# Performance work log

Measured on AMD Instinct MI355X. Metric: run time of the kernel, lower is better.

Reference implementation:

```python
import jax, jax.numpy as jnp
import numpy as np

N_NODES = 50000
N_EDGES = 800000
IN_FEATS = 256
HIDDEN = 128
OUT_FEATS = 64


def setup_inputs() -> dict:
    key = jax.random.key(0)
    k1, k2, k3, k4, k5 = jax.random.split(key, 5)
    x = jax.random.normal(k1, (N_NODES, IN_FEATS), dtype=jnp.float32)
    src = jax.random.randint(k2, (N_EDGES,), 0, N_NODES, dtype=jnp.int64)
    dst = jax.random.randint(k3, (N_EDGES,), 0, N_NODES, dtype=jnp.int64)
    # Glorot-ish init for linear weights (DGL GraphConv uses xavier_uniform)
    W1 = jax.random.normal(k4, (IN_FEATS, HIDDEN), dtype=jnp.float32) / np.sqrt(IN_FEATS)
    W2 = jax.random.normal(k5, (HIDDEN, OUT_FEATS), dtype=jnp.float32) / np.sqrt(HIDDEN)
    b1 = jnp.zeros((HIDDEN,), dtype=jnp.float32)
    b2 = jnp.zeros((OUT_FEATS,), dtype=jnp.float32)
    return {"x": x, "src": src, "dst": dst, "W1": W1, "b1": b1, "W2": W2, "b2": b2}


def _norms(src, dst, n_nodes):
    ones = jnp.ones(src.shape[0], dtype=jnp.float32)
    deg_out = jax.ops.segment_sum(ones, src, num_segments=n_nodes)
    deg_in = jax.ops.segment_sum(ones, dst, num_segments=n_nodes)
    # DGL clamps zero degrees to 1 to avoid inf
    norm_src = jnp.power(jnp.clip(deg_out, 1.0, None), -0.5)  # [N]
    norm_dst = jnp.power(jnp.clip(deg_in, 1.0, None), -0.5)   # [N]
    return norm_src, norm_dst


def _gcn_layer(h, W, b, src, dst, norm_src, norm_dst, n_nodes):
    # norm='both': D_dst^{-1/2} A D_src^{-1/2} (h W) + b
    # multiply by W first (in_feats >= out_feats -> cheaper aggregation)
    m = (h * norm_src[:, None]) @ W            # [N, out]
    agg = jax.ops.segment_sum(m[src], dst, num_segments=n_nodes)  # [N, out]
    return agg * norm_dst[:, None] + b


def reference(x, src, dst, W1, b1, W2, b2):
    n = x.shape[0]
    norm_src, norm_dst = _norms(src, dst, n)
    h = _gcn_layer(x, W1, b1, src, dst, norm_src, norm_dst, n)
    h = jax.nn.relu(h)
    h = _gcn_layer(h, W2, b2, src, dst, norm_src, norm_dst, n)
    return h
```

## Files before the change

kernel.cpp:

```cpp
#include <hip/hip_runtime.h>

#define N_NODES 50000
#define N_EDGES 800000
#define IN_FEATS 256
#define HIDDEN 128
#define OUT_FEATS 64

#define NB 8192
#define NRANGE 7
#define NBT (NRANGE * NB)
#define NCHUNK 64
#define EPC 12500
#define HBLK (NRANGE * NCHUNK)
#define ROWBLK ((N_NODES + 63) / 64)
#define G1BLK (ROWBLK * 2)

typedef _Float16 f16;
typedef _Float16 f16x2 __attribute__((ext_vector_type(2)));
typedef _Float16 f16x8 __attribute__((ext_vector_type(8)));
typedef float f32x4 __attribute__((ext_vector_type(4)));

__global__ __launch_bounds__(256) void hist_gemm_kernel(
    const int* __restrict__ src, const int* __restrict__ dst,
    unsigned* __restrict__ hist_src, unsigned* __restrict__ hist_dst,
    const float* __restrict__ W1, const float* __restrict__ W2,
    f16* __restrict__ W2T, const float* __restrict__ x,
    f16* __restrict__ m1) {
  __shared__ __align__(16) unsigned smem[8448];
  if (blockIdx.x < HBLK) {
    unsigned* ls = smem;
    unsigned* ld2 = smem + NB / 2;
    const int r = blockIdx.x % NRANGE;
    const int c = blockIdx.x / NRANGE;
    const int lo = r * NB;
    for (int i = threadIdx.x; i < NB / 2; i += 256) {
      ls[i] = 0;
      ld2[i] = 0;
    }
    __syncthreads();
    const int4* s4 = (const int4*)(src + c * EPC);
    const int4* d4 = (const int4*)(dst + c * EPC);
    for (int i = threadIdx.x; i < EPC / 4; i += 256) {
      int4 s = s4[i];
      int4 d = d4[i];
      unsigned b;
      b = (unsigned)(s.x - lo); if (b < NB) atomicAdd(&ls[b >> 1], 1u << ((b & 1) << 4));
      b = (unsigned)(s.y - lo); if (b < NB) atomicAdd(&ls[b >> 1], 1u << ((b & 1) << 4));
      b = (unsigned)(s.z - lo); if (b < NB) atomicAdd(&ls[b >> 1], 1u << ((b & 1) << 4));
      b = (unsigned)(s.w - lo); if (b < NB) atomicAdd(&ls[b >> 1], 1u << ((b & 1) << 4));
      b = (unsigned)(d.x - lo); if (b < NB) atomicAdd(&ld2[b >> 1], 1u << ((b & 1) << 4));
      b = (unsigned)(d.y - lo); if (b < NB) atomicAdd(&ld2[b >> 1], 1u << ((b & 1) << 4));
      b = (unsigned)(d.z - lo); if (b < NB) atomicAdd(&ld2[b >> 1], 1u << ((b & 1) << 4));
      b = (unsigned)(d.w - lo); if (b < NB) atomicAdd(&ld2[b >> 1], 1u << ((b & 1) << 4));
    }
    __syncthreads();
    unsigned* hs = hist_src + ((long)c * NBT + lo) / 2;
    unsigned* hd = hist_dst + ((long)c * NBT + lo) / 2;
    for (int i = threadIdx.x; i < NB / 2; i += 256) {
      hs[i] = ls[i];
      hd[i] = ld2[i];
    }
    if (blockIdx.x < 32) {
      int j = blockIdx.x * 256 + threadIdx.x;
      int n = j >> 7, k = j & 127;
      W2T[j] = (f16)W2[k * 64 + n];
    }
  } else {
    f16* Bs = (f16*)smem;
    constexpr int KP = IN_FEATS + 8;
    const int bid = blockIdx.x - HBLK;
    const int cb = bid & 1;
    const int rb = bid >> 1;
    const int col0 = cb * 64;
    const int wave = threadIdx.x >> 6;
    const int lane = threadIdx.x & 63;
    const int m = lane & 15;
    const int q = lane >> 4;
    const int row0 = rb * 64 + wave * 16;

    for (int idx = threadIdx.x; idx < 64 * (IN_FEATS / 2); idx += 256) {
      int k2 = idx >> 6;
      int n = idx & 63;
      float a0 = W1[(2 * k2) * HIDDEN + col0 + n];
      float a1 = W1[(2 * k2 + 1) * HIDDEN + col0 + n];
      f16x2 pk;
      pk[0] = (f16)a0;
      pk[1] = (f16)a1;
      *(f16x2*)(Bs + n * KP + 2 * k2) = pk;
    }
    __syncthreads();

    const int ra = min(row0 + m, N_NODES - 1);
    f32x4 acc[4];
#pragma unroll
    for (int t = 0; t < 4; ++t) acc[t] = (f32x4){0.f, 0.f, 0.f, 0.f};

#pragma unroll
    for (int ki = 0; ki < IN_FEATS / 32; ++ki) {
      const int kb = ki * 32 + q * 8;
      const float* p = x + (long)ra * IN_FEATS + kb;
      float4 u0 = *(const float4*)p;
      float4 u1 = *(const float4*)(p + 4);
      f16x8 a;
      a[0] = (f16)u0.x; a[1] = (f16)u0.y;
      a[2] = (f16)u0.z; a[3] = (f16)u0.w;
      a[4] = (f16)u1.x; a[5] = (f16)u1.y;
      a[6] = (f16)u1.z; a[7] = (f16)u1.w;
#pragma unroll
      for (int t = 0; t < 4; ++t) {
        f16x8 bfr = *(const f16x8*)(Bs + (t * 16 + m) * KP + kb);
        acc[t] = __builtin_amdgcn_mfma_f32_16x16x32_f16(a, bfr, acc[t], 0, 0, 0);
      }
    }

#pragma unroll
    for (int rr = 0; rr < 4; ++rr) {
      int row = row0 + q * 4 + rr;
      if (row < N_NODES) {
#pragma unroll
        for (int t = 0; t < 4; ++t)
          m1[(long)row * HIDDEN + col0 + t * 16 + m] = (f16)acc[t][rr];
      }
    }
  }
}

__global__ __launch_bounds__(256) void reduce_kernel(
    const unsigned* __restrict__ hist_src, unsigned* __restrict__ hist_dst,
    int* __restrict__ deg_in, float* __restrict__ norm_src,
    float* __restrict__ norm_dst, int* __restrict__ partial) {
  const unsigned short* hs = (const unsigned short*)hist_src;
  unsigned short* hd = (unsigned short*)hist_dst;
  int n = blockIdx.x * 256 + threadIdx.x;
  int run = 0;
  if (n < N_NODES) {
    int so = 0;
#pragma unroll 8
    for (int c = 0; c < NCHUNK; ++c) so += hs[(long)c * NBT + n];
    norm_src[n] = rsqrtf((float)max(so, 1));
#pragma unroll 8
    for (int c = 0; c < NCHUNK; ++c) {
      int t = hd[(long)c * NBT + n];
      hd[(long)c * NBT + n] = (unsigned short)run;
      run += t;
    }
    deg_in[n] = run;
    norm_dst[n] = rsqrtf((float)max(run, 1));
  }
  __shared__ int sd[256];
  sd[threadIdx.x] = run;
  __syncthreads();
  for (int s = 128; s > 0; s >>= 1) {
    if (threadIdx.x < s) sd[threadIdx.x] += sd[threadIdx.x + s];
    __syncthreads();
  }
  if (threadIdx.x == 0) partial[blockIdx.x] = sd[0];
}

__global__ __launch_bounds__(256) void scan3(const int* __restrict__ deg,
                                             const int* __restrict__ partial,
                                             int* __restrict__ rowptr) {
  __shared__ int sd[256];
  __shared__ int sp[256];
  const int w = blockIdx.x;
  int pv = (threadIdx.x < 196) ? partial[threadIdx.x] : 0;
  sp[threadIdx.x] = pv;
  __syncthreads();
  for (int off = 1; off < 256; off <<= 1) {
    int t = sp[threadIdx.x] +
            ((threadIdx.x >= off) ? sp[threadIdx.x - off] : 0);
    __syncthreads();
    sp[threadIdx.x] = t;
    __syncthreads();
  }
  const int base = (w == 0) ? 0 : sp[w - 1];
  int i = w * 256 + threadIdx.x;
  int v = (i < N_NODES) ? deg[i] : 0;
  sd[threadIdx.x] = v;
  __syncthreads();
  for (int off = 1; off < 256; off <<= 1) {
    int t = sd[threadIdx.x] +
            ((threadIdx.x >= off) ? sd[threadIdx.x - off] : 0);
    __syncthreads();
    sd[threadIdx.x] = t;
    __syncthreads();
  }
  if (i < N_NODES) rowptr[i] = base + sd[threadIdx.x] - v;
  if (w == 0 && threadIdx.x == 0) rowptr[N_NODES] = N_EDGES;
}

__global__ __launch_bounds__(256) void fill_csr(
    const int* __restrict__ src, const int* __restrict__ dst,
    const int* __restrict__ rowptr, const unsigned* __restrict__ pref32,
    int* __restrict__ col) {
  __shared__ int cur[NB];
  const unsigned short* pref = (const unsigned short*)pref32;
  const int r = blockIdx.x % NRANGE;
  const int c = blockIdx.x / NRANGE;
  const int lo = r * NB;
  for (int i = threadIdx.x; i < NB; i += 256) {
    int n = lo + i;
    cur[i] = (n < N_NODES) ? rowptr[n] + pref[(long)c * NBT + n] : 0;
  }
  __syncthreads();
  const int4* s4 = (const int4*)(src + c * EPC);
  const int4* d4 = (const int4*)(dst + c * EPC);
  for (int i = threadIdx.x; i < EPC / 4; i += 256) {
    int4 s = s4[i];
    int4 d = d4[i];
    unsigned b;
    b = (unsigned)(d.x - lo);
    if (b < NB) col[atomicAdd(&cur[b], 1)] = s.x;
    b = (unsigned)(d.y - lo);
    if (b < NB) col[atomicAdd(&cur[b], 1)] = s.y;
    b = (unsigned)(d.z - lo);
    if (b < NB) col[atomicAdd(&cur[b], 1)] = s.z;
    b = (unsigned)(d.w - lo);
    if (b < NB) col[atomicAdd(&cur[b], 1)] = s.w;
  }
}

template <int K, int NC, int TN, bool FP32IN>
__global__ __launch_bounds__(256) void gemm_mfma(
    const void* __restrict__ Xv, const f16* __restrict__ WT,
    const float* __restrict__ ns, f16* __restrict__ Mout) {
  constexpr int KI = K / 32;
  constexpr int COLBLK = NC / (TN * 16);
  constexpr int KP = K + 8;
  __shared__ f16 Bs[TN * 16 * KP];

  const int cb = blockIdx.x % COLBLK;
  const int rb = blockIdx.x / COLBLK;
  const int col0 = cb * TN * 16;
  const int wave = threadIdx.x >> 6;
  const int lane = threadIdx.x & 63;
  const int m = lane & 15;
  const int q = lane >> 4;
  const int row0 = rb * 64 + wave * 16;

  for (int idx = threadIdx.x; idx < TN * 16 * (K / 8); idx += 256) {
    int n = idx / (K / 8);
    int kk = idx % (K / 8);
    *(f16x8*)(Bs + n * KP + kk * 8) =
        *(const f16x8*)(WT + (long)(col0 + n) * K + kk * 8);
  }
  __syncthreads();

  const int ra = min(row0 + m, N_NODES - 1);
  const float s = FP32IN ? ns[ra] : 0.f;

  f32x4 acc[TN];
#pragma unroll
  for (int t = 0; t < TN; ++t) acc[t] = (f32x4){0.f, 0.f, 0.f, 0.f};

#pragma unroll
  for (int ki = 0; ki < KI; ++ki) {
    const int kb = ki * 32 + q * 8;
    f16x8 a;
    if (FP32IN) {
      const float* X = (const float*)Xv;
      const float* p = X + (long)ra * K + kb;
      float4 u0 = *(const float4*)p;
      float4 u1 = *(const float4*)(p + 4);
      a[0] = (f16)(u0.x * s); a[1] = (f16)(u0.y * s);
      a[2] = (f16)(u0.z * s); a[3] = (f16)(u0.w * s);
      a[4] = (f16)(u1.x * s); a[5] = (f16)(u1.y * s);
      a[6] = (f16)(u1.z * s); a[7] = (f16)(u1.w * s);
    } else {
      const f16* X = (const f16*)Xv;
      a = *(const f16x8*)(X + (long)ra * K + kb);
    }
#pragma unroll
    for (int t = 0; t < TN; ++t) {
      f16x8 b = *(const f16x8*)(Bs + (t * 16 + m) * KP + kb);
      acc[t] = __builtin_amdgcn_mfma_f32_16x16x32_f16(a, b, acc[t], 0, 0, 0);
    }
  }

#pragma unroll
  for (int r = 0; r < 4; ++r) {
    int row = row0 + q * 4 + r;
    if (row < N_NODES) {
#pragma unroll
      for (int t = 0; t < TN; ++t)
        Mout[(long)row * NC + col0 + t * 16 + m] = (f16)acc[t][r];
    }
  }
}

__global__ __launch_bounds__(256) void gather1_kernel(
    const f16* __restrict__ M, const int* __restrict__ rowptr,
    const int* __restrict__ col, const float* __restrict__ nd,
    const float* __restrict__ ns, const float* __restrict__ b,
    f16* __restrict__ out) {
  constexpr int LPR = 16;
  constexpr int EPW = 64 / LPR;
  const int wave = threadIdx.x >> 6;
  const int lane = threadIdx.x & 63;
  const int eg = lane / LPR;
  const int t = lane % LPR;
  const int n = blockIdx.x * 4 + wave;
  if (n >= N_NODES) return;
  const int beg = rowptr[n];
  const int end = rowptr[n + 1];

  float acc[8];
#pragma unroll
  for (int j = 0; j < 8; ++j) acc[j] = 0.f;

  int i = beg + eg;
  for (; i + EPW < end; i += 2 * EPW) {
    int s0 = col[i];
    int s1 = col[i + EPW];
    float n0 = ns[s0];
    float n1 = ns[s1];
    f16x8 v0 = *(const f16x8*)(M + (long)s0 * HIDDEN + t * 8);
    f16x8 v1 = *(const f16x8*)(M + (long)s1 * HIDDEN + t * 8);
#pragma unroll
    for (int j = 0; j < 8; ++j)
      acc[j] += n0 * (float)v0[j] + n1 * (float)v1[j];
  }
  if (i < end) {
    int s0 = col[i];
    float n0 = ns[s0];
    f16x8 v0 = *(const f16x8*)(M + (long)s0 * HIDDEN + t * 8);
#pragma unroll
    for (int j = 0; j < 8; ++j) acc[j] += n0 * (float)v0[j];
  }

#pragma unroll
  for (int m2 = LPR; m2 < 64; m2 <<= 1)
#pragma unroll
    for (int j = 0; j < 8; ++j) acc[j] += __shfl_xor(acc[j], m2, 64);

  if (eg == 0) {
    float s = nd[n];
    float sn = ns[n];
    float4 bb0 = *(const float4*)(b + t * 8);
    float4 bb1 = *(const float4*)(b + t * 8 + 4);
    f16x8 o;
    o[0] = (f16)(fmaxf(acc[0] * s + bb0.x, 0.f) * sn);
    o[1] = (f16)(fmaxf(acc[1] * s + bb0.y, 0.f) * sn);
    o[2] = (f16)(fmaxf(acc[2] * s + bb0.z, 0.f) * sn);
    o[3] = (f16)(fmaxf(acc[3] * s + bb0.w, 0.f) * sn);
    o[4] = (f16)(fmaxf(acc[4] * s + bb1.x, 0.f) * sn);
    o[5] = (f16)(fmaxf(acc[5] * s + bb1.y, 0.f) * sn);
    o[6] = (f16)(fmaxf(acc[6] * s + bb1.z, 0.f) * sn);
    o[7] = (f16)(fmaxf(acc[7] * s + bb1.w, 0.f) * sn);
    *(f16x8*)(out + (long)n * HIDDEN + t * 8) = o;
  }
}

__global__ __launch_bounds__(256) void gather2_kernel(
    const f16* __restrict__ M, const int* __restrict__ rowptr,
    const int* __restrict__ col, const float* __restrict__ nd,
    const float* __restrict__ b, float* __restrict__ out) {
  constexpr int LPR = 8;
  constexpr int EPW = 64 / LPR;
  const int wave = threadIdx.x >> 6;
  const int lane = threadIdx.x & 63;
  const int eg = lane / LPR;
  const int t = lane % LPR;
  const int n = blockIdx.x * 4 + wave;
  if (n >= N_NODES) return;
  const int beg = rowptr[n];
  const int end = rowptr[n + 1];

  float acc[8];
#pragma unroll
  for (int j = 0; j < 8; ++j) acc[j] = 0.f;

  int i = beg + eg;
  for (; i + EPW < end; i += 2 * EPW) {
    int s0 = col[i];
    int s1 = col[i + EPW];
    f16x8 v0 = *(const f16x8*)(M + (long)s0 * OUT_FEATS + t * 8);
    f16x8 v1 = *(const f16x8*)(M + (long)s1 * OUT_FEATS + t * 8);
#pragma unroll
    for (int j = 0; j < 8; ++j) acc[j] += (float)v0[j] + (float)v1[j];
  }
  if (i < end) {
    int s0 = col[i];
    f16x8 v0 = *(const f16x8*)(M + (long)s0 * OUT_FEATS + t * 8);
#pragma unroll
    for (int j = 0; j < 8; ++j) acc[j] += (float)v0[j];
  }

#pragma unroll
  for (int m2 = LPR; m2 < 64; m2 <<= 1)
#pragma unroll
    for (int j = 0; j < 8; ++j) acc[j] += __shfl_xor(acc[j], m2, 64);

  if (eg == 0) {
    float s = nd[n];
    float4 bb0 = *(const float4*)(b + t * 8);
    float4 bb1 = *(const float4*)(b + t * 8 + 4);
    float4 o0, o1;
    o0.x = acc[0] * s + bb0.x;
    o0.y = acc[1] * s + bb0.y;
    o0.z = acc[2] * s + bb0.z;
    o0.w = acc[3] * s + bb0.w;
    o1.x = acc[4] * s + bb1.x;
    o1.y = acc[5] * s + bb1.y;
    o1.z = acc[6] * s + bb1.z;
    o1.w = acc[7] * s + bb1.w;
    *(float4*)(out + (long)n * OUT_FEATS + t * 8) = o0;
    *(float4*)(out + (long)n * OUT_FEATS + t * 8 + 4) = o1;
  }
}

extern "C" void kernel_launch(void* const* d_in, const int* in_sizes, int n_in,
                              void* d_out, int out_size, void* d_ws,
                              size_t ws_size, hipStream_t stream) {
  const float* x = (const float*)d_in[0];
  const int* src = (const int*)d_in[1];
  const int* dst = (const int*)d_in[2];
  const float* W1 = (const float*)d_in[3];
  const float* b1 = (const float*)d_in[4];
  const float* W2 = (const float*)d_in[5];
  const float* b2 = (const float*)d_in[6];
  float* out = (float*)d_out;

  int* wi = (int*)d_ws;
  int* partial = wi;
  int* rowptr = wi + 256;
  int* deg_in = wi + 50260;
  int* col = wi + 100260;
  float* wf = (float*)d_ws + 900260;
  float* norm_src = wf;
  float* norm_dst = wf + 50000;
  f16* fh = (f16*)(wf + 100000);
  f16* W2T = fh;
  f16* m1 = fh + 64 * 128;
  f16* h1p = m1 + (long)50048 * 128;
  f16* m2 = h1p + (long)50048 * 128;

  unsigned* hist_src = (unsigned*)h1p;
  unsigned* hist_dst = hist_src + (long)NCHUNK * NBT / 2;

  const int nb_nodes = (N_NODES + 255) / 256;

  hist_gemm_kernel<<<HBLK + G1BLK, 256, 0, stream>>>(
      src, dst, hist_src, hist_dst, W1, W2, W2T, x, m1);
  reduce_kernel<<<nb_nodes, 256, 0, stream>>>(hist_src, hist_dst, deg_in,
                                              norm_src, norm_dst, partial);
  scan3<<<nb_nodes, 256, 0, stream>>>(deg_in, partial, rowptr);
  fill_csr<<<HBLK, 256, 0, stream>>>(src, dst, rowptr, hist_dst, col);

  gather1_kernel<<<(N_NODES + 3) / 4, 256, 0, stream>>>(m1, rowptr, col,
                                                        norm_dst, norm_src, b1,
                                                        h1p);

  gemm_mfma<HIDDEN, OUT_FEATS, 4, false>
      <<<ROWBLK, 256, 0, stream>>>(h1p, W2T, norm_src, m2);
  gather2_kernel<<<(N_NODES + 3) / 4, 256, 0, stream>>>(m2, rowptr, col,
                                                        norm_dst, b2, out);
}
```

Before: 235.3 us.

## Reuse x row tile across both W1 column halves in fused hist-GEMM kernel

Each GEMM block now handles all 128 output columns for its 64 rows. The x row is loaded and converted to fp16 once into registers, and the block loops over the two 64-column halves of W1, restaging each half into shared memory. This halves the x reads and the block count for the first GEMM. The shared-memory layout drops its padding in favour of an XOR swizzle to avoid bank conflicts. In exchange, each block serializes two W1 staging passes with extra barriers, and more registers are held for the A fragments.

Result: faster. 226.8 us (-3.6%).

```diff
diff --git a/kernel.cpp b/kernel.cpp
--- a/kernel.cpp
+++ b/kernel.cpp
@@ -13,7 +13,6 @@
 #define EPC 12500
 #define HBLK (NRANGE * NCHUNK)
 #define ROWBLK ((N_NODES + 63) / 64)
-#define G1BLK (ROWBLK * 2)
 
 typedef _Float16 f16;
 typedef _Float16 f16x2 __attribute__((ext_vector_type(2)));
@@ -26,7 +25,7 @@
     const float* __restrict__ W1, const float* __restrict__ W2,
     f16* __restrict__ W2T, const float* __restrict__ x,
     f16* __restrict__ m1) {
-  __shared__ __align__(16) unsigned smem[8448];
+  __shared__ __align__(16) unsigned smem[8192];
   if (blockIdx.x < HBLK) {
     unsigned* ls = smem;
     unsigned* ld2 = smem + NB / 2;
@@ -66,60 +65,69 @@
       W2T[j] = (f16)W2[k * 64 + n];
     }
   } else {
-    f16* Bs = (f16*)smem;
-    constexpr int KP = IN_FEATS + 8;
-    const int bid = blockIdx.x - HBLK;
-    const int cb = bid & 1;
-    const int rb = bid >> 1;
-    const int col0 = cb * 64;
+    char* BsBytes = (char*)smem;
+    const int rb = blockIdx.x - HBLK;
     const int wave = threadIdx.x >> 6;
     const int lane = threadIdx.x & 63;
     const int m = lane & 15;
     const int q = lane >> 4;
     const int row0 = rb * 64 + wave * 16;
-
-    for (int idx = threadIdx.x; idx < 64 * (IN_FEATS / 2); idx += 256) {
-      int k2 = idx >> 6;
-      int n = idx & 63;
-      float a0 = W1[(2 * k2) * HIDDEN + col0 + n];
-      float a1 = W1[(2 * k2 + 1) * HIDDEN + col0 + n];
-      f16x2 pk;
-      pk[0] = (f16)a0;
-      pk[1] = (f16)a1;
-      *(f16x2*)(Bs + n * KP + 2 * k2) = pk;
-    }
-    __syncthreads();
-
     const int ra = min(row0 + m, N_NODES - 1);
-    f32x4 acc[4];
-#pragma unroll
-    for (int t = 0; t < 4; ++t) acc[t] = (f32x4){0.f, 0.f, 0.f, 0.f};
-
-#pragma unroll
-    for (int ki = 0; ki < IN_FEATS / 32; ++ki) {
-      const int kb = ki * 32 + q * 8;
-      const float* p = x + (long)ra * IN_FEATS + kb;
+
+    f16x8 a[8];
+#pragma unroll
+    for (int ki = 0; ki < 8; ++ki) {
+      const float* p = x + (long)ra * IN_FEATS + ki * 32 + q * 8;
       float4 u0 = *(const float4*)p;
       float4 u1 = *(const float4*)(p + 4);
-      f16x8 a;
-      a[0] = (f16)u0.x; a[1] = (f16)u0.y;
-      a[2] = (f16)u0.z; a[3] = (f16)u0.w;
-      a[4] = (f16)u1.x; a[5] = (f16)u1.y;
-      a[6] = (f16)u1.z; a[7] = (f16)u1.w;
-#pragma unroll
-      for (int t = 0; t < 4; ++t) {
-        f16x8 bfr = *(const f16x8*)(Bs + (t * 16 + m) * KP + kb);
-        acc[t] = __builtin_amdgcn_mfma_f32_16x16x32_f16(a, bfr, acc[t], 0, 0, 0);
+      a[ki][0] = (f16)u0.x; a[ki][1] = (f16)u0.y;
+      a[ki][2] = (f16)u0.z; a[ki][3] = (f16)u0.w;
+      a[ki][4] = (f16)u1.x; a[ki][5] = (f16)u1.y;
+      a[ki][6] = (f16)u1.z; a[ki][7] = (f16)u1.w;
+    }
+
+    for (int h = 0; h < 2; ++h) {
+      const int col0 = h * 64;
+      for (int idx = threadIdx.x; idx < 64 * 128; idx += 256) {
+        int k2 = idx >> 6;
+        int n = idx & 63;
+        float a0 = W1[(2 * k2) * HIDDEN + col0 + n];
+        float a1 = W1[(2 * k2 + 1) * HIDDEN + col0 + n];
+        f16x2 pk;
+        pk[0] = (f16)a0;
+        pk[1] = (f16)a1;
+        unsigned bo = (unsigned)(n * 512 + 4 * k2);
+        bo ^= (unsigned)((n & 7) << 4);
+        *(f16x2*)(BsBytes + bo) = pk;
       }
-    }
-
-#pragma unroll
-    for (int rr = 0; rr < 4; ++rr) {
-      int row = row0 + q * 4 + rr;
-      if (row < N_NODES) {
-#pragma unroll
-        for (int t = 0; t < 4; ++t)
-          m1[(long)row * HIDDEN + col0 + t * 16 + m] = (f16)acc[t][rr];
+      __syncthreads();
+
+      f32x4 acc[4];
+#pragma unroll
+      for (int t = 0; t < 4; ++t) acc[t] = (f32x4){0.f, 0.f, 0.f, 0.f};
+
+#pragma unroll
+      for (int ki = 0; ki < 8; ++ki) {
+        const int kb2 = (ki * 32 + q * 8) * 2;
+#pragma unroll
+        for (int t = 0; t < 4; ++t) {
+          int nrow = t * 16 + m;
+          unsigned bo = (unsigned)(nrow * 512 + kb2);
+          bo ^= (unsigned)((nrow & 7) << 4);
+          f16x8 bfr = *(const f16x8*)(BsBytes + bo);
+          acc[t] = __builtin_amdgcn_mfma_f32_16x16x32_f16(a[ki], bfr, acc[t], 0, 0, 0);
+        }
+      }
+      __syncthreads();
+
+#pragma unroll
+      for (int rr = 0; rr < 4; ++rr) {
+        int row = row0 + q * 4 + rr;
+        if (row < N_NODES) {
+#pragma unroll
+          for (int t = 0; t < 4; ++t)
+            m1[(long)row * HIDDEN + col0 + t * 16 + m] = (f16)acc[t][rr];
+        }
       }
     }
   }
@@ -440,7 +448,7 @@
 
   const int nb_nodes = (N_NODES + 255) / 256;
 
-  hist_gemm_kernel<<<HBLK + G1BLK, 256, 0, stream>>>(
+  hist_gemm_kernel<<<HBLK + ROWBLK, 256, 0, stream>>>(
       src, dst, hist_src, hist_dst, W1, W2, W2T, x, m1);
   reduce_kernel<<<nb_nodes, 256, 0, stream>>>(hist_src, hist_dst, deg_in,
                                               norm_src, norm_dst, partial);
```
